# Performance work log

Hardware: AMD Instinct MI355X
Metric: run time of the kernel (lower is better)

The kernel has to match this reference:

```python
import jax, jax.numpy as jnp
import numpy as np
import math

B, S, D, H, NB = 32, 512, 512, 8, 2
DK = D // H
DF = 4 * D
EPS = 1e-8


def layer_norm(x, gamma, beta):
    # Matches torch: unbiased std (ddof=1), divide by (std + eps)
    mean = jnp.mean(x, axis=-1, keepdims=True)
    std = jnp.sqrt(jnp.var(x, axis=-1, keepdims=True, ddof=1))
    return gamma * (x - mean) / (std + EPS) + beta


def block(x, wq, bq, wk, bk, wv, bv, wr, br, ga, ba, wc1, bc1, wc2, bc2, gf, bf):
    # --- attention with ReLU-gated Q/K/V ---
    Q = jax.nn.relu(x @ wq.T + bq)  # [B,S,D]
    K = jax.nn.relu(x @ wk.T + bk)
    V = jax.nn.relu(x @ wv.T + bv)
    # chunk along last dim -> heads; head-major stacking is equivalent to this reshape
    Qh = Q.reshape(B, S, H, DK)
    Kh = K.reshape(B, S, H, DK)
    Vh = V.reshape(B, S, H, DK)
    scores = jnp.einsum('bqhd,bkhd->bhqk', Qh, Kh) / math.sqrt(DK)
    w = jax.nn.softmax(scores, axis=-1)
    out = jnp.einsum('bhqk,bkhd->bqhd', w, Vh).reshape(B, S, D)
    out = out + jax.nn.relu(x @ wr.T + br)
    out = layer_norm(out, ga, ba)
    # --- conv1d (kernel=1) feed-forward ---
    h = jax.nn.relu(out @ wc1.T + bc1)  # [B,S,4D]
    y = h @ wc2.T + bc2                 # [B,S,D]
    y = layer_norm(y + out, gf, bf)
    return y


def setup_inputs() -> dict:
    key = jax.random.key(0)
    ks = jax.random.split(key, 8)
    std = 0.01
    inp = {
        'x': jax.random.normal(ks[0], (B, S, D), jnp.float32),
        'wq': jax.random.normal(ks[1], (NB, D, D), jnp.float32) * std,
        'bq': jnp.zeros((NB, D), jnp.float32),
        'wk': jax.random.normal(ks[2], (NB, D, D), jnp.float32) * std,
        'bk': jnp.zeros((NB, D), jnp.float32),
        'wv': jax.random.normal(ks[3], (NB, D, D), jnp.float32) * std,
        'bv': jnp.zeros((NB, D), jnp.float32),
        'wr': jax.random.normal(ks[4], (NB, D, D), jnp.float32) * std,
        'br': jnp.zeros((NB, D), jnp.float32),
        'g_attn': jnp.ones((NB, D), jnp.float32),
        'b_attn': jnp.zeros((NB, D), jnp.float32),
        'wc1': jax.random.normal(ks[5], (NB, DF, D), jnp.float32) * (1.0 / math.sqrt(D)),
        'bc1': jnp.zeros((NB, DF), jnp.float32),
        'wc2': jax.random.normal(ks[6], (NB, D, DF), jnp.float32) * (1.0 / math.sqrt(DF)),
        'bc2': jnp.zeros((NB, D), jnp.float32),
        'g_ffn': jnp.ones((NB, D), jnp.float32),
        'b_ffn': jnp.zeros((NB, D), jnp.float32),
    }
    return inp


def reference(x, wq, bq, wk, bk, wv, bv, wr, br, g_attn, b_attn,
              wc1, bc1, wc2, bc2, g_ffn, b_ffn):
    enc = x
    for i in range(NB):
        enc = block(enc, wq[i], bq[i], wk[i], bk[i], wv[i], bv[i], wr[i], br[i],
                    g_attn[i], b_attn[i], wc1[i], bc1[i], wc2[i], bc2[i],
                    g_ffn[i], b_ffn[i])
    return enc
```

## Files before the change

### kernel.cpp

```cpp
#include <hip/hip_runtime.h>

typedef unsigned short u16;
typedef __bf16 bf16x8 __attribute__((ext_vector_type(8)));
typedef float f32x4 __attribute__((ext_vector_type(4)));
typedef unsigned short ushort8 __attribute__((ext_vector_type(8)));

__device__ __forceinline__ void gload_lds16(const void* g, void* l) {
  __builtin_amdgcn_global_load_lds(
      (const __attribute__((address_space(1))) void*)g,
      (__attribute__((address_space(3))) void*)l, 16, 0, 0);
}

__device__ __forceinline__ u16 f2bf(float f) {
  unsigned int u = __builtin_bit_cast(unsigned int, f);
  u = (u + 0x7fffu + ((u >> 16) & 1u)) >> 16;
  return (u16)u;
}
__device__ __forceinline__ u16 f2bf_trunc(float f) {
  return (u16)(__builtin_bit_cast(unsigned int, f) >> 16);
}
__device__ __forceinline__ float bf2f(u16 u) {
  unsigned int v = (unsigned int)u << 16;
  return __builtin_bit_cast(float, v);
}

__global__ void castk(const float* __restrict__ in, u16* __restrict__ out, int n,
                      float scale) {
  size_t i = ((size_t)blockIdx.x * 256 + threadIdx.x) * 8;
  if (i >= (size_t)n) return;
  const float4* p = (const float4*)(in + i);
  float4 a = p[0], b = p[1];
  ushort8 o;
  o[0] = f2bf(a.x * scale); o[1] = f2bf(a.y * scale);
  o[2] = f2bf(a.z * scale); o[3] = f2bf(a.w * scale);
  o[4] = f2bf(b.x * scale); o[5] = f2bf(b.y * scale);
  o[6] = f2bf(b.z * scale); o[7] = f2bf(b.w * scale);
  *(ushort8*)(out + i) = o;
}

__global__ void castw4(const float* __restrict__ w0, const float* __restrict__ w1,
                       const float* __restrict__ w2, const float* __restrict__ w3,
                       u16* __restrict__ out) {
  size_t idx = ((size_t)blockIdx.x * 256 + threadIdx.x) * 8;
  int i = (int)(idx >> 20);
  int j = (int)((idx >> 18) & 3);
  int e = (int)(idx & 262143);
  const float* src = (j == 0) ? w0 : (j == 1) ? w1 : (j == 2) ? w2 : w3;
  float scale = (j == 0) ? 0.125f : 1.0f;
  const float4* p = (const float4*)(src + (size_t)i * 262144 + e);
  float4 a = p[0], b = p[1];
  ushort8 o;
  o[0] = f2bf(a.x * scale); o[1] = f2bf(a.y * scale);
  o[2] = f2bf(a.z * scale); o[3] = f2bf(a.w * scale);
  o[4] = f2bf(b.x * scale); o[5] = f2bf(b.y * scale);
  o[6] = f2bf(b.z * scale); o[7] = f2bf(b.w * scale);
  *(ushort8*)(out + idx) = o;
}

__global__ void biasg(const float* __restrict__ b0, const float* __restrict__ b1,
                      const float* __restrict__ b2, const float* __restrict__ b3,
                      float* __restrict__ out) {
  int idx = blockIdx.x * 256 + threadIdx.x;
  int i = idx >> 11, j = (idx >> 9) & 3, c = idx & 511;
  const float* src = (j == 0) ? b0 : (j == 1) ? b1 : (j == 2) ? b2 : b3;
  float v = src[i * 512 + c];
  out[idx] = (j == 0) ? v * 0.125f : v;
}

template<int RELU, int WVT>
__global__ __launch_bounds__(256, 4)
void gemm97(const u16* __restrict__ A, const u16* __restrict__ W,
            const float* __restrict__ bias, u16* __restrict__ C,
            u16* __restrict__ VT, int M, int N, int K)
{
  __shared__ char lds[32768];
  char* ABase = lds;
  char* BBase = lds + 16384;

  const int tid = threadIdx.x, w = tid >> 6, l = tid & 63;
  const int l15 = l & 15, lh = l >> 4;
  const int nbn = N >> 7;
  const int p = blockIdx.x;
  const int bm = (p & 7) * 16 + (p >> 3) / nbn;
  const int bn = (p >> 3) % nbn;
  const int wm = w >> 1, wn = w & 1;
  const int NT = K >> 6;

  const int srow = l >> 3;
  const int scol = ((l & 7) ^ srow) << 3;
  const u16* aG = A + (size_t)(bm * 128 + srow) * K + scol;
  const u16* bG = W + (size_t)(bn * 128 + srow) * K + scol;

  auto stage = [&](int t) {
#pragma unroll
    for (int i = 0; i < 4; ++i) {
      int c = w * 4 + i;
      gload_lds16(aG + (size_t)(c * 8) * K + t * 64, ABase + c * 1024);
      gload_lds16(bG + (size_t)(c * 8) * K + t * 64, BBase + c * 1024);
    }
  };

  f32x4 acc[4][4] = {};

  for (int t = 0; t < NT; ++t) {
    __syncthreads();
    stage(t);
    __syncthreads();
    bf16x8 a[4], b[4];
#pragma unroll
    for (int kk = 0; kk < 2; ++kk) {
#pragma unroll
      for (int mf = 0; mf < 4; ++mf) {
        int row = wm * 64 + mf * 16 + l15;
        a[mf] = *(const bf16x8*)(ABase + row * 128 +
                 ((kk * 64 + lh * 16) ^ ((row & 7) << 4)));
      }
#pragma unroll
      for (int nf = 0; nf < 4; ++nf) {
        int row = wn * 64 + nf * 16 + l15;
        b[nf] = *(const bf16x8*)(BBase + row * 128 +
                 ((kk * 64 + lh * 16) ^ ((row & 7) << 4)));
      }
      __builtin_amdgcn_s_setprio(1);
#pragma unroll
      for (int mf = 0; mf < 4; ++mf)
#pragma unroll
        for (int nf = 0; nf < 4; ++nf)
          acc[mf][nf] = __builtin_amdgcn_mfma_f32_16x16x32_bf16(a[mf], b[nf], acc[mf][nf], 0, 0, 0);
      __builtin_amdgcn_s_setprio(0);
    }
  }

  __syncthreads();
  char* Ct = (char*)lds;
  const int rowL = wm * 64 + (lh << 2);
  const int colL = wn * 64 + l15;
  const bool dovt = WVT && (bn >= 8) && (bn < 12);
  float bv[4];
#pragma unroll
  for (int nf = 0; nf < 4; ++nf) bv[nf] = bias[bn * 128 + colL + nf * 16];

  if (!dovt) {
#pragma unroll
    for (int mf = 0; mf < 4; ++mf)
#pragma unroll
      for (int nf = 0; nf < 4; ++nf)
#pragma unroll
        for (int r = 0; r < 4; ++r) {
          float v = acc[mf][nf][r] + bv[nf];
          if (RELU) v = fmaxf(v, 0.f);
          int m = rowL + mf * 16 + r, n = colL + nf * 16;
          *(u16*)(Ct + m * 256 + ((n * 2) ^ ((m & 7) << 4))) = f2bf(v);
        }
    __syncthreads();
#pragma unroll
    for (int pass = 0; pass < 8; ++pass) {
      int row = pass * 16 + (tid >> 4);
      int c16 = tid & 15;
      bf16x8 vv = *(const bf16x8*)(Ct + row * 256 + ((c16 * 16) ^ ((row & 7) << 4)));
      *(bf16x8*)(&C[(size_t)(bm * 128 + row) * N + bn * 128 + c16 * 8]) = vv;
    }
  } else {
#pragma unroll
    for (int mf = 0; mf < 4; ++mf)
#pragma unroll
      for (int nf = 0; nf < 4; ++nf)
#pragma unroll
        for (int r = 0; r < 4; ++r) {
          float v = acc[mf][nf][r] + bv[nf];
          if (RELU) v = fmaxf(v, 0.f);
          int m = rowL + mf * 16 + r, d = colL + nf * 16;
          *(u16*)(Ct + d * 256 + ((m * 2) ^ ((d & 7) << 4))) = f2bf(v);
        }
    __syncthreads();
    const int batch = bm >> 2;
#pragma unroll
    for (int pass = 0; pass < 8; ++pass) {
      int dL = pass * 16 + (tid >> 4);
      int m16 = tid & 15;
      bf16x8 vv = *(const bf16x8*)(Ct + dL * 256 + ((m16 * 16) ^ ((dL & 7) << 4)));
      int head = (bn - 8) * 2 + (dL >> 6);
      int vtr = (batch * 8 + head) * 64 + (dL & 63);
      *(bf16x8*)(&VT[(size_t)vtr * 512 + (bm & 3) * 128 + m16 * 8]) = vv;
    }
  }
}

__global__ __launch_bounds__(256, 2)
void attn_kernel(const u16* __restrict__ qkvr, const u16* __restrict__ VT,
                 u16* __restrict__ F)
{
  const int D4 = 2048;
  __shared__ u16 Qs[128 * 64];
  __shared__ u16 Ks[2][64 * 64];
  __shared__ u16 Vs[2][64 * 64];
  __shared__ u16 Ps[128 * 64];

  const int tid = threadIdx.x, w = tid >> 6, l = tid & 63;
  const int bh = blockIdx.x & 255, qt = blockIdx.x >> 8;
  const int b = bh >> 3, h = bh & 7;
  const int lr = l >> 3, lc = ((l & 7) ^ lr) << 3;
  const int l15 = l & 15, lh = l >> 4;

  const u16* qG = qkvr + (size_t)(b * 512 + qt * 128) * D4 + h * 64 + lc;
#pragma unroll
  for (int i = 0; i < 4; ++i) {
    int c = w * 4 + i;
    gload_lds16(qG + (size_t)(c * 8 + lr) * D4, &Qs[c * 512]);
  }

  const u16* kG = qkvr + (size_t)(b * 512) * D4 + 512 + h * 64 + lc;
  const u16* vG = VT + (size_t)(bh * 64) * 512 + lc;

  auto stageKV = [&](int kt) {
    const int bsel = kt & 1;
#pragma unroll
    for (int i = 0; i < 2; ++i) {
      int c = w * 2 + i;
      gload_lds16(kG + (size_t)(kt * 64 + c * 8 + lr) * D4, &Ks[bsel][c * 512]);
      gload_lds16(vG + (size_t)(c * 8 + lr) * 512 + kt * 64, &Vs[bsel][c * 512]);
    }
  };
  stageKV(0);

  f32x4 o_acc[2][4] = {};
  float psum[2][4] = {};

  for (int kt = 0; kt < 8; ++kt) {
    __syncthreads();
    if (kt < 7) stageKV(kt + 1);
    const char* Kb = (const char*)Ks[kt & 1];
    const char* Vb = (const char*)Vs[kt & 1];

    f32x4 sacc[2][4] = {};
#pragma unroll
    for (int kk = 0; kk < 2; ++kk) {
      bf16x8 qa[2];
#pragma unroll
      for (int qq = 0; qq < 2; ++qq) {
        int qrow = w * 32 + qq * 16 + l15;
        qa[qq] = *(const bf16x8*)((const char*)Qs + qrow * 128 +
                  ((kk * 64 + (lh << 4)) ^ ((qrow & 7) << 4)));
      }
#pragma unroll
      for (int ni = 0; ni < 4; ++ni) {
        int krow = ni * 16 + l15;
        bf16x8 kb = *(const bf16x8*)(Kb + krow * 128 +
                    ((kk * 64 + (lh << 4)) ^ ((krow & 7) << 4)));
#pragma unroll
        for (int qq = 0; qq < 2; ++qq)
          sacc[qq][ni] = __builtin_amdgcn_mfma_f32_16x16x32_bf16(qa[qq], kb, sacc[qq][ni], 0, 0, 0);
      }
    }

#pragma unroll
    for (int qq = 0; qq < 2; ++qq)
#pragma unroll
      for (int r = 0; r < 4; ++r) {
        float p0 = __expf(sacc[qq][0][r]);
        float p1 = __expf(sacc[qq][1][r]);
        float p2 = __expf(sacc[qq][2][r]);
        float p3 = __expf(sacc[qq][3][r]);
        psum[qq][r] += (p0 + p1) + (p2 + p3);
        int q = w * 32 + qq * 16 + (lh << 2) + r;
        int sw = (q & 7) << 4;
        int col = l15 * 2;
        char* pb = (char*)Ps + q * 128;
        *(u16*)(pb + ((0  + col) ^ sw)) = f2bf_trunc(p0);
        *(u16*)(pb + ((32 + col) ^ sw)) = f2bf_trunc(p1);
        *(u16*)(pb + ((64 + col) ^ sw)) = f2bf_trunc(p2);
        *(u16*)(pb + ((96 + col) ^ sw)) = f2bf_trunc(p3);
      }

#pragma unroll
    for (int kk = 0; kk < 2; ++kk) {
      bf16x8 pa[2];
#pragma unroll
      for (int qq = 0; qq < 2; ++qq) {
        int qrow = w * 32 + qq * 16 + l15;
        pa[qq] = *(const bf16x8*)((const char*)Ps + qrow * 128 +
                  ((kk * 64 + (lh << 4)) ^ ((qrow & 7) << 4)));
      }
#pragma unroll
      for (int ni = 0; ni < 4; ++ni) {
        int d = ni * 16 + l15;
        bf16x8 vb = *(const bf16x8*)(Vb + d * 128 +
                    ((kk * 64 + (lh << 4)) ^ ((d & 7) << 4)));
#pragma unroll
        for (int qq = 0; qq < 2; ++qq)
          o_acc[qq][ni] = __builtin_amdgcn_mfma_f32_16x16x32_bf16(pa[qq], vb, o_acc[qq][ni], 0, 0, 0);
      }
    }
  }

  float lsum[2][4];
#pragma unroll
  for (int qq = 0; qq < 2; ++qq)
#pragma unroll
    for (int r = 0; r < 4; ++r) {
      float t = psum[qq][r];
#pragma unroll
      for (int m = 1; m < 16; m <<= 1) t += __shfl_xor(t, m);
      lsum[qq][r] = 1.f / t;
    }

#pragma unroll
  for (int qq = 0; qq < 2; ++qq)
#pragma unroll
    for (int ni = 0; ni < 4; ++ni) {
      int d = ni * 16 + l15;
#pragma unroll
      for (int r = 0; r < 4; ++r) {
        float v = o_acc[qq][ni][r] * lsum[qq][r];
        int q = w * 32 + qq * 16 + (lh << 2) + r;
        *(u16*)((char*)Ps + q * 128 + ((d * 2) ^ ((q & 7) << 4))) = f2bf(v);
      }
    }
  __syncthreads();
  const u16* Rbase = qkvr + (size_t)(b * 512 + qt * 128) * D4 + 1536 + h * 64;
  u16* Fbase = F + (size_t)(b * 512 + qt * 128) * 512 + h * 64;
#pragma unroll
  for (int pass = 0; pass < 4; ++pass) {
    int row = pass * 32 + (tid >> 3), c8 = tid & 7;
    ushort8 lv = *(const ushort8*)((char*)Ps + row * 128 + ((c8 * 16) ^ ((row & 7) << 4)));
    ushort8 rv = *(const ushort8*)(Rbase + (size_t)row * D4 + c8 * 8);
    ushort8 o;
#pragma unroll
    for (int j = 0; j < 8; ++j) o[j] = f2bf(bf2f(lv[j]) + bf2f(rv[j]));
    *(ushort8*)(Fbase + (size_t)row * 512 + c8 * 8) = o;
  }
}

template<int HAS_RES, int OUT_F32>
__global__ __launch_bounds__(256)
void ln_bf(const u16* __restrict__ in, const u16* __restrict__ res,
           const float* __restrict__ gamma, const float* __restrict__ beta,
           u16* __restrict__ outb, float* __restrict__ outf)
{
  const int l = threadIdx.x & 63;
  const size_t row = (size_t)blockIdx.x * 4 + (threadIdx.x >> 6);
  ushort8 iv = *(const ushort8*)(in + row * 512 + l * 8);
  float x[8];
#pragma unroll
  for (int j = 0; j < 8; ++j) x[j] = bf2f(iv[j]);
  if (HAS_RES) {
    ushort8 rv = *(const ushort8*)(res + row * 512 + l * 8);
#pragma unroll
    for (int j = 0; j < 8; ++j) x[j] += bf2f(rv[j]);
  }
  float s = 0.f, ss = 0.f;
#pragma unroll
  for (int j = 0; j < 8; ++j) { s += x[j]; ss += x[j] * x[j]; }
#pragma unroll
  for (int m = 1; m < 64; m <<= 1) { s += __shfl_xor(s, m); ss += __shfl_xor(ss, m); }
  float mean = s * (1.f / 512.f);
  float var = fmaxf((ss - 512.f * mean * mean) * (1.f / 511.f), 0.f);
  float inv = 1.f / (sqrtf(var) + 1e-8f);
  const float4* g4 = (const float4*)gamma;
  const float4* b4 = (const float4*)beta;
  float4 g0 = g4[l * 2], g1 = g4[l * 2 + 1];
  float4 b0 = b4[l * 2], b1 = b4[l * 2 + 1];
  float gg[8] = {g0.x, g0.y, g0.z, g0.w, g1.x, g1.y, g1.z, g1.w};
  float bb[8] = {b0.x, b0.y, b0.z, b0.w, b1.x, b1.y, b1.z, b1.w};
  float y[8];
#pragma unroll
  for (int j = 0; j < 8; ++j) y[j] = gg[j] * (x[j] - mean) * inv + bb[j];
  ushort8 o;
#pragma unroll
  for (int j = 0; j < 8; ++j) o[j] = f2bf(y[j]);
  *(ushort8*)(outb + row * 512 + l * 8) = o;
  if (OUT_F32) {
    float4* o4 = (float4*)(outf + row * 512);
    o4[l * 2]     = make_float4(y[0], y[1], y[2], y[3]);
    o4[l * 2 + 1] = make_float4(y[4], y[5], y[6], y[7]);
  }
}

extern "C" void kernel_launch(void* const* d_in, const int* in_sizes, int n_in,
                              void* d_out, int out_size, void* d_ws, size_t ws_size,
                              hipStream_t stream)
{
  const int B = 32, S = 512, D = 512, NB = 2, DF = 2048;
  const int M = B * S;

  const float* x   = (const float*)d_in[0];
  const float* ga  = (const float*)d_in[9];
  const float* ba  = (const float*)d_in[10];
  const float* wc1 = (const float*)d_in[11];
  const float* bc1 = (const float*)d_in[12];
  const float* wc2 = (const float*)d_in[13];
  const float* bc2 = (const float*)d_in[14];
  const float* gf  = (const float*)d_in[15];
  const float* bfp = (const float*)d_in[16];

  char* ws = (char*)d_ws;
  u16*   curb = (u16*)(ws + 0);
  u16*   qkvr = (u16*)(ws + 16777216);
  u16*   F    = (u16*)(ws + 83886080);
  u16*   Hg   = (u16*)(ws + 100663296);
  u16*   VT   = (u16*)(ws + 117440512);
  u16*   w4b  = (u16*)(ws + 134217728);
  u16*   wc1b = (u16*)(ws + 138412032);
  u16*   wc2b = (u16*)(ws + 142606336);
  float* b4   = (float*)(ws + 146800640);
  u16*   Ih   = qkvr;
  u16*   Y    = F;

  castk<<<M * D / 2048, 256, 0, stream>>>(x, curb, M * D, 1.0f);
  castw4<<<1024, 256, 0, stream>>>((const float*)d_in[1], (const float*)d_in[3],
                                   (const float*)d_in[5], (const float*)d_in[7], w4b);
  biasg<<<16, 256, 0, stream>>>((const float*)d_in[2], (const float*)d_in[4],
                                (const float*)d_in[6], (const float*)d_in[8], b4);
  castk<<<NB * DF * D / 2048, 256, 0, stream>>>(wc1, wc1b, NB * DF * D, 1.0f);
  castk<<<NB * DF * D / 2048, 256, 0, stream>>>(wc2, wc2b, NB * DF * D, 1.0f);

  for (int i = 0; i < NB; ++i) {
    const size_t wfo = (size_t)i * DF * D;
    gemm97<1, 1><<<128 * 16, 256, 0, stream>>>(curb, w4b + (size_t)i * 1048576,
                                               b4 + i * 2048, qkvr, VT, M, 2048, 512);
    attn_kernel<<<4 * 256, 256, 0, stream>>>(qkvr, VT, F);
    ln_bf<0, 0><<<M / 4, 256, 0, stream>>>(F, nullptr, ga + i * D, ba + i * D, Hg, nullptr);
    gemm97<1, 0><<<128 * 16, 256, 0, stream>>>(Hg, wc1b + wfo, bc1 + i * DF,
                                               Ih, nullptr, M, 2048, 512);
    gemm97<0, 0><<<128 * 4, 256, 0, stream>>>(Ih, wc2b + wfo, bc2 + i * D,
                                              Y, nullptr, M, 512, 2048);
    if (i == NB - 1)
      ln_bf<1, 1><<<M / 4, 256, 0, stream>>>(Y, Hg, gf + i * D, bfp + i * D,
                                             curb, (float*)d_out);
    else
      ln_bf<1, 0><<<M / 4, 256, 0, stream>>>(Y, Hg, gf + i * D, bfp + i * D,
                                             curb, nullptr);
  }
}
```

Before: 358.7 us.

## Add 256x256-tile 8-wave GEMM with phased LDS pipeline for QKV and FFN1

```diff
diff --git a/kernel.cpp b/kernel.cpp
--- a/kernel.cpp
+++ b/kernel.cpp
@@ -68,6 +68,175 @@
 }
 
 template<int RELU, int WVT>
+__global__ __launch_bounds__(512, 1)
+void gemm8p(const u16* __restrict__ A, const u16* __restrict__ W,
+            const float* __restrict__ bias, u16* __restrict__ C,
+            u16* __restrict__ VT, int M, int N, int K)
+{
+  __shared__ char lds[131072];
+
+  const int tid = threadIdx.x, w = tid >> 6, l = tid & 63;
+  const int l15 = l & 15, lh = l >> 4;
+  const int nbn = N >> 8;
+  const int p = blockIdx.x;
+  const int g0 = (p & 7) * ((gridDim.x >> 3) / nbn) * nbn + (p >> 3);
+  const int bm = g0 / nbn, bn = g0 % nbn;
+  const int wm = w >> 2, wn = w & 3;
+  const int NI = K >> 7;
+
+  const int srow = l >> 3;
+  const int scol = ((l & 7) ^ srow) << 3;
+
+  auto stA = [&](int t, int h) {
+#pragma unroll
+    for (int j = 0; j < 2; ++j) {
+      int c = w * 2 + j;
+      gload_lds16(A + (size_t)(bm * 256 + h * 128 + c * 8 + srow) * K + t * 64 + scol,
+                  lds + (t & 1) * 32768 + h * 16384 + c * 1024);
+    }
+  };
+  auto stB = [&](int t, int h) {
+#pragma unroll
+    for (int j = 0; j < 2; ++j) {
+      int c = w * 2 + j;
+      gload_lds16(W + (size_t)(bn * 256 + h * 128 + c * 8 + srow) * K + t * 64 + scol,
+                  lds + 65536 + (t & 1) * 32768 + h * 16384 + c * 1024);
+    }
+  };
+
+  f32x4 acc[8][4] = {};
+  bf16x8 a[2][8], b[2][4];
+
+  auto rdA = [&](int buf, int kk, bf16x8* dst) {
+#pragma unroll
+    for (int mf = 0; mf < 8; ++mf) {
+      int r = mf * 16 + l15;
+      dst[mf] = *(const bf16x8*)(lds + buf * 32768 + wm * 16384 + r * 128 +
+                 ((kk * 64 + lh * 16) ^ ((r & 7) << 4)));
+    }
+  };
+  auto rdB = [&](int buf, int kk, bf16x8* dst) {
+#pragma unroll
+    for (int nf = 0; nf < 4; ++nf) {
+      int r = (wn & 1) * 64 + nf * 16 + l15;
+      dst[nf] = *(const bf16x8*)(lds + 65536 + buf * 32768 + (wn >> 1) * 16384 +
+                 r * 128 + ((kk * 64 + lh * 16) ^ ((r & 7) << 4)));
+    }
+  };
+
+#define PH_MID()                                              \
+  __builtin_amdgcn_sched_barrier(0);                          \
+  __builtin_amdgcn_s_barrier();                               \
+  asm volatile("s_waitcnt lgkmcnt(0)" ::: "memory");          \
+  __builtin_amdgcn_sched_barrier(0)
+#define PH_END()                                              \
+  __builtin_amdgcn_sched_barrier(0);                          \
+  __builtin_amdgcn_s_barrier();                               \
+  __builtin_amdgcn_sched_barrier(0)
+#define QMFMA(KK, MH)                                         \
+  { __builtin_amdgcn_s_setprio(1);                            \
+    _Pragma("unroll") for (int mf = 0; mf < 4; ++mf)          \
+    _Pragma("unroll") for (int nf = 0; nf < 4; ++nf)          \
+      acc[(MH) * 4 + mf][nf] = __builtin_amdgcn_mfma_f32_16x16x32_bf16( \
+          a[KK][(MH) * 4 + mf], b[KK][nf], acc[(MH) * 4 + mf][nf], 0, 0, 0); \
+    __builtin_amdgcn_s_setprio(0); }
+
+  stA(0, 0); stA(0, 1); stB(0, 0); stB(0, 1); stA(1, 0); stA(1, 1);
+  asm volatile("s_waitcnt vmcnt(4)" ::: "memory");
+  __builtin_amdgcn_s_barrier();
+  __builtin_amdgcn_sched_barrier(0);
+
+  for (int i = 0; i < NI; ++i) {
+    const int t0 = 2 * i, t1 = 2 * i + 1;
+    const bool g = (i + 1 < NI);
+    rdA(0, 0, a[0]); rdB(0, 0, b[0]);
+    stB(t1, 0);
+    PH_MID(); QMFMA(0, 0); PH_END();
+    rdA(0, 1, a[1]); rdB(0, 1, b[1]);
+    stB(t1, 1);
+    PH_MID(); QMFMA(0, 1); PH_END();
+    if (g) stA(t0 + 2, 0);
+    PH_MID(); QMFMA(1, 0); PH_END();
+    if (g) stA(t0 + 2, 1);
+    PH_MID(); QMFMA(1, 1);
+    __builtin_amdgcn_sched_barrier(0);
+    if (g) asm volatile("s_waitcnt vmcnt(4)" ::: "memory");
+    else   asm volatile("s_waitcnt vmcnt(0)" ::: "memory");
+    PH_END();
+    rdA(1, 0, a[0]); rdB(1, 0, b[0]);
+    if (g) stB(t0 + 2, 0);
+    PH_MID(); QMFMA(0, 0); PH_END();
+    rdA(1, 1, a[1]); rdB(1, 1, b[1]);
+    if (g) stB(t0 + 2, 1);
+    PH_MID(); QMFMA(0, 1); PH_END();
+    if (g) stA(t0 + 3, 0);
+    PH_MID(); QMFMA(1, 0); PH_END();
+    if (g) stA(t0 + 3, 1);
+    PH_MID(); QMFMA(1, 1);
+    __builtin_amdgcn_sched_barrier(0);
+    if (g) asm volatile("s_waitcnt vmcnt(4)" ::: "memory");
+    PH_END();
+  }
+#undef PH_MID
+#undef PH_END
+#undef QMFMA
+
+  __syncthreads();
+  char* Ct = (char*)lds;
+  const int rowL = wm * 128 + (lh << 2);
+  const int colL = wn * 64 + l15;
+  const bool dovt = WVT && (bn == 4 || bn == 5);
+  float bv[4];
+#pragma unroll
+  for (int nf = 0; nf < 4; ++nf) bv[nf] = bias[bn * 256 + colL + nf * 16];
+
+  if (!dovt) {
+#pragma unroll
+    for (int mi = 0; mi < 8; ++mi)
+#pragma unroll
+      for (int nf = 0; nf < 4; ++nf)
+#pragma unroll
+        for (int r = 0; r < 4; ++r) {
+          float v = acc[mi][nf][r] + bv[nf];
+          if (RELU) v = fmaxf(v, 0.f);
+          int m = rowL + mi * 16 + r, n = colL + nf * 16;
+          *(u16*)(Ct + m * 512 + ((n * 2) ^ ((m & 7) << 4))) = f2bf(v);
+        }
+    __syncthreads();
+#pragma unroll
+    for (int pass = 0; pass < 16; ++pass) {
+      int row = pass * 16 + (tid >> 5);
+      int c16 = tid & 31;
+      bf16x8 vv = *(const bf16x8*)(Ct + row * 512 + ((c16 * 16) ^ ((row & 7) << 4)));
+      *(bf16x8*)(&C[(size_t)(bm * 256 + row) * N + bn * 256 + c16 * 8]) = vv;
+    }
+  } else {
+#pragma unroll
+    for (int mi = 0; mi < 8; ++mi)
+#pragma unroll
+      for (int nf = 0; nf < 4; ++nf)
+#pragma unroll
+        for (int r = 0; r < 4; ++r) {
+          float v = acc[mi][nf][r] + bv[nf];
+          if (RELU) v = fmaxf(v, 0.f);
+          int m = rowL + mi * 16 + r, d = colL + nf * 16;
+          *(u16*)(Ct + d * 512 + ((m * 2) ^ ((d & 7) << 4))) = f2bf(v);
+        }
+    __syncthreads();
+    const int batch = bm >> 1;
+#pragma unroll
+    for (int pass = 0; pass < 16; ++pass) {
+      int dL = pass * 16 + (tid >> 5);
+      int m16 = tid & 31;
+      bf16x8 vv = *(const bf16x8*)(Ct + dL * 512 + ((m16 * 16) ^ ((dL & 7) << 4)));
+      int head = (bn - 4) * 4 + (dL >> 6);
+      int vtr = (batch * 8 + head) * 64 + (dL & 63);
+      *(bf16x8*)(&VT[(size_t)vtr * 512 + (bm & 1) * 256 + m16 * 8]) = vv;
+    }
+  }
+}
+
+template<int RELU, int WVT>
 __global__ __launch_bounds__(256, 4)
 void gemm97(const u16* __restrict__ A, const u16* __restrict__ W,
             const float* __restrict__ bias, u16* __restrict__ C,
@@ -135,54 +304,28 @@
   char* Ct = (char*)lds;
   const int rowL = wm * 64 + (lh << 2);
   const int colL = wn * 64 + l15;
-  const bool dovt = WVT && (bn >= 8) && (bn < 12);
   float bv[4];
 #pragma unroll
   for (int nf = 0; nf < 4; ++nf) bv[nf] = bias[bn * 128 + colL + nf * 16];
 
-  if (!dovt) {
-#pragma unroll
-    for (int mf = 0; mf < 4; ++mf)
-#pragma unroll
-      for (int nf = 0; nf < 4; ++nf)
-#pragma unroll
-        for (int r = 0; r < 4; ++r) {
-          float v = acc[mf][nf][r] + bv[nf];
-          if (RELU) v = fmaxf(v, 0.f);
-          int m = rowL + mf * 16 + r, n = colL + nf * 16;
-          *(u16*)(Ct + m * 256 + ((n * 2) ^ ((m & 7) << 4))) = f2bf(v);
-        }
-    __syncthreads();
-#pragma unroll
-    for (int pass = 0; pass < 8; ++pass) {
-      int row = pass * 16 + (tid >> 4);
-      int c16 = tid & 15;
-      bf16x8 vv = *(const bf16x8*)(Ct + row * 256 + ((c16 * 16) ^ ((row & 7) << 4)));
-      *(bf16x8*)(&C[(size_t)(bm * 128 + row) * N + bn * 128 + c16 * 8]) = vv;
-    }
-  } else {
-#pragma unroll
-    for (int mf = 0; mf < 4; ++mf)
-#pragma unroll
-      for (int nf = 0; nf < 4; ++nf)
-#pragma unroll
-        for (int r = 0; r < 4; ++r) {
-          float v = acc[mf][nf][r] + bv[nf];
-          if (RELU) v = fmaxf(v, 0.f);
-          int m = rowL + mf * 16 + r, d = colL + nf * 16;
-          *(u16*)(Ct + d * 256 + ((m * 2) ^ ((d & 7) << 4))) = f2bf(v);
-        }
-    __syncthreads();
-    const int batch = bm >> 2;
-#pragma unroll
-    for (int pass = 0; pass < 8; ++pass) {
-      int dL = pass * 16 + (tid >> 4);
-      int m16 = tid & 15;
-      bf16x8 vv = *(const bf16x8*)(Ct + dL * 256 + ((m16 * 16) ^ ((dL & 7) << 4)));
-      int head = (bn - 8) * 2 + (dL >> 6);
-      int vtr = (batch * 8 + head) * 64 + (dL & 63);
-      *(bf16x8*)(&VT[(size_t)vtr * 512 + (bm & 3) * 128 + m16 * 8]) = vv;
-    }
+#pragma unroll
+  for (int mf = 0; mf < 4; ++mf)
+#pragma unroll
+    for (int nf = 0; nf < 4; ++nf)
+#pragma unroll
+      for (int r = 0; r < 4; ++r) {
+        float v = acc[mf][nf][r] + bv[nf];
+        if (RELU) v = fmaxf(v, 0.f);
+        int m = rowL + mf * 16 + r, n = colL + nf * 16;
+        *(u16*)(Ct + m * 256 + ((n * 2) ^ ((m & 7) << 4))) = f2bf(v);
+      }
+  __syncthreads();
+#pragma unroll
+  for (int pass = 0; pass < 8; ++pass) {
+    int row = pass * 16 + (tid >> 4);
+    int c16 = tid & 15;
+    bf16x8 vv = *(const bf16x8*)(Ct + row * 256 + ((c16 * 16) ^ ((row & 7) << 4)));
+    *(bf16x8*)(&C[(size_t)(bm * 128 + row) * N + bn * 128 + c16 * 8]) = vv;
   }
 }
 
@@ -416,12 +559,12 @@
 
   for (int i = 0; i < NB; ++i) {
     const size_t wfo = (size_t)i * DF * D;
-    gemm97<1, 1><<<128 * 16, 256, 0, stream>>>(curb, w4b + (size_t)i * 1048576,
-                                               b4 + i * 2048, qkvr, VT, M, 2048, 512);
+    gemm8p<1, 1><<<512, 512, 0, stream>>>(curb, w4b + (size_t)i * 1048576,
+                                          b4 + i * 2048, qkvr, VT, M, 2048, 512);
     attn_kernel<<<4 * 256, 256, 0, stream>>>(qkvr, VT, F);
     ln_bf<0, 0><<<M / 4, 256, 0, stream>>>(F, nullptr, ga + i * D, ba + i * D, Hg, nullptr);
-    gemm97<1, 0><<<128 * 16, 256, 0, stream>>>(Hg, wc1b + wfo, bc1 + i * DF,
-                                               Ih, nullptr, M, 2048, 512);
+    gemm8p<1, 0><<<512, 512, 0, stream>>>(Hg, wc1b + wfo, bc1 + i * DF,
+                                          Ih, nullptr, M, 2048, 512);
     gemm97<0, 0><<<128 * 4, 256, 0, stream>>>(Ih, wc2b + wfo, bc2 + i * D,
                                               Y, nullptr, M, 512, 2048);
     if (i == NB - 1)
```

New measurement: 478.2 us. 33.3% more time.

## Add double-buffered K=32 GEMM for QKV and FFN1, skip unused final bf16 output

Applied to the files above, without the earlier changes.

```diff
diff --git a/kernel.cpp b/kernel.cpp
--- a/kernel.cpp
+++ b/kernel.cpp
@@ -69,9 +69,128 @@
 
 template<int RELU, int WVT>
 __global__ __launch_bounds__(256, 4)
+void gemmDB(const u16* __restrict__ A, const u16* __restrict__ W,
+            const float* __restrict__ bias, u16* __restrict__ C,
+            u16* __restrict__ VT, int M, int N, int K)
+{
+  __shared__ char lds[32768];
+
+  const int tid = threadIdx.x, w = tid >> 6, l = tid & 63;
+  const int l15 = l & 15, lh = l >> 4;
+  const int nbn = N >> 7;
+  const int p = blockIdx.x;
+  const int bm = (p & 7) * 16 + (p >> 3) / nbn;
+  const int bn = (p >> 3) % nbn;
+  const int wm = w >> 1, wn = w & 1;
+  const int NT = K >> 5;
+
+  const int srow = l >> 2;
+  const int scol = ((l & 3) ^ ((l >> 3) & 3)) << 3;
+  const u16* aG = A + (size_t)(bm * 128 + srow) * K + scol;
+  const u16* bG = W + (size_t)(bn * 128 + srow) * K + scol;
+
+  auto stage = [&](int t) {
+    char* base = lds + (t & 1) * 16384;
+#pragma unroll
+    for (int i = 0; i < 2; ++i) {
+      int c = i * 4 + w;
+      gload_lds16(aG + (size_t)(c * 16) * K + t * 32, base + c * 1024);
+      gload_lds16(bG + (size_t)(c * 16) * K + t * 32, base + 8192 + c * 1024);
+    }
+  };
+
+  f32x4 acc[4][4] = {};
+  const int sw = ((l15 >> 1) & 3) << 4;
+
+  stage(0);
+  for (int t = 0; t < NT; ++t) {
+    asm volatile("s_waitcnt vmcnt(0)" ::: "memory");
+    __builtin_amdgcn_s_barrier();
+    __builtin_amdgcn_sched_barrier(0);
+    if (t + 1 < NT) stage(t + 1);
+
+    const char* Ab = lds + (t & 1) * 16384;
+    const char* Bb = Ab + 8192;
+    bf16x8 a[4], b[4];
+#pragma unroll
+    for (int mf = 0; mf < 4; ++mf) {
+      int row = wm * 64 + mf * 16 + l15;
+      a[mf] = *(const bf16x8*)(Ab + row * 64 + ((lh << 4) ^ sw));
+    }
+#pragma unroll
+    for (int nf = 0; nf < 4; ++nf) {
+      int row = wn * 64 + nf * 16 + l15;
+      b[nf] = *(const bf16x8*)(Bb + row * 64 + ((lh << 4) ^ sw));
+    }
+    __builtin_amdgcn_s_setprio(1);
+#pragma unroll
+    for (int mf = 0; mf < 4; ++mf)
+#pragma unroll
+      for (int nf = 0; nf < 4; ++nf)
+        acc[mf][nf] = __builtin_amdgcn_mfma_f32_16x16x32_bf16(a[mf], b[nf], acc[mf][nf], 0, 0, 0);
+    __builtin_amdgcn_s_setprio(0);
+  }
+
+  __syncthreads();
+  char* Ct = (char*)lds;
+  const int rowL = wm * 64 + (lh << 2);
+  const int colL = wn * 64 + l15;
+  const bool dovt = WVT && (bn >= 8) && (bn < 12);
+  float bv[4];
+#pragma unroll
+  for (int nf = 0; nf < 4; ++nf) bv[nf] = bias[bn * 128 + colL + nf * 16];
+
+  if (!dovt) {
+#pragma unroll
+    for (int mf = 0; mf < 4; ++mf)
+#pragma unroll
+      for (int nf = 0; nf < 4; ++nf)
+#pragma unroll
+        for (int r = 0; r < 4; ++r) {
+          float v = acc[mf][nf][r] + bv[nf];
+          if (RELU) v = fmaxf(v, 0.f);
+          int m = rowL + mf * 16 + r, n = colL + nf * 16;
+          *(u16*)(Ct + m * 256 + ((n * 2) ^ ((m & 7) << 4))) = f2bf(v);
+        }
+    __syncthreads();
+#pragma unroll
+    for (int pass = 0; pass < 8; ++pass) {
+      int row = pass * 16 + (tid >> 4);
+      int c16 = tid & 15;
+      bf16x8 vv = *(const bf16x8*)(Ct + row * 256 + ((c16 * 16) ^ ((row & 7) << 4)));
+      *(bf16x8*)(&C[(size_t)(bm * 128 + row) * N + bn * 128 + c16 * 8]) = vv;
+    }
+  } else {
+#pragma unroll
+    for (int mf = 0; mf < 4; ++mf)
+#pragma unroll
+      for (int nf = 0; nf < 4; ++nf)
+#pragma unroll
+        for (int r = 0; r < 4; ++r) {
+          float v = acc[mf][nf][r] + bv[nf];
+          if (RELU) v = fmaxf(v, 0.f);
+          int m = rowL + mf * 16 + r, d = colL + nf * 16;
+          *(u16*)(Ct + d * 256 + ((m * 2) ^ ((d & 7) << 4))) = f2bf(v);
+        }
+    __syncthreads();
+    const int batch = bm >> 2;
+#pragma unroll
+    for (int pass = 0; pass < 8; ++pass) {
+      int dL = pass * 16 + (tid >> 4);
+      int m16 = tid & 15;
+      bf16x8 vv = *(const bf16x8*)(Ct + dL * 256 + ((m16 * 16) ^ ((dL & 7) << 4)));
+      int head = (bn - 8) * 2 + (dL >> 6);
+      int vtr = (batch * 8 + head) * 64 + (dL & 63);
+      *(bf16x8*)(&VT[(size_t)vtr * 512 + (bm & 3) * 128 + m16 * 8]) = vv;
+    }
+  }
+}
+
+template<int RELU>
+__global__ __launch_bounds__(256, 4)
 void gemm97(const u16* __restrict__ A, const u16* __restrict__ W,
             const float* __restrict__ bias, u16* __restrict__ C,
-            u16* __restrict__ VT, int M, int N, int K)
+            int M, int N, int K)
 {
   __shared__ char lds[32768];
   char* ABase = lds;
@@ -135,54 +254,28 @@
   char* Ct = (char*)lds;
   const int rowL = wm * 64 + (lh << 2);
   const int colL = wn * 64 + l15;
-  const bool dovt = WVT && (bn >= 8) && (bn < 12);
   float bv[4];
 #pragma unroll
   for (int nf = 0; nf < 4; ++nf) bv[nf] = bias[bn * 128 + colL + nf * 16];
 
-  if (!dovt) {
-#pragma unroll
-    for (int mf = 0; mf < 4; ++mf)
-#pragma unroll
-      for (int nf = 0; nf < 4; ++nf)
-#pragma unroll
-        for (int r = 0; r < 4; ++r) {
-          float v = acc[mf][nf][r] + bv[nf];
-          if (RELU) v = fmaxf(v, 0.f);
-          int m = rowL + mf * 16 + r, n = colL + nf * 16;
-          *(u16*)(Ct + m * 256 + ((n * 2) ^ ((m & 7) << 4))) = f2bf(v);
-        }
-    __syncthreads();
-#pragma unroll
-    for (int pass = 0; pass < 8; ++pass) {
-      int row = pass * 16 + (tid >> 4);
-      int c16 = tid & 15;
-      bf16x8 vv = *(const bf16x8*)(Ct + row * 256 + ((c16 * 16) ^ ((row & 7) << 4)));
-      *(bf16x8*)(&C[(size_t)(bm * 128 + row) * N + bn * 128 + c16 * 8]) = vv;
-    }
-  } else {
-#pragma unroll
-    for (int mf = 0; mf < 4; ++mf)
-#pragma unroll
-      for (int nf = 0; nf < 4; ++nf)
-#pragma unroll
-        for (int r = 0; r < 4; ++r) {
-          float v = acc[mf][nf][r] + bv[nf];
-          if (RELU) v = fmaxf(v, 0.f);
-          int m = rowL + mf * 16 + r, d = colL + nf * 16;
-          *(u16*)(Ct + d * 256 + ((m * 2) ^ ((d & 7) << 4))) = f2bf(v);
-        }
-    __syncthreads();
-    const int batch = bm >> 2;
-#pragma unroll
-    for (int pass = 0; pass < 8; ++pass) {
-      int dL = pass * 16 + (tid >> 4);
-      int m16 = tid & 15;
-      bf16x8 vv = *(const bf16x8*)(Ct + dL * 256 + ((m16 * 16) ^ ((dL & 7) << 4)));
-      int head = (bn - 8) * 2 + (dL >> 6);
-      int vtr = (batch * 8 + head) * 64 + (dL & 63);
-      *(bf16x8*)(&VT[(size_t)vtr * 512 + (bm & 3) * 128 + m16 * 8]) = vv;
-    }
+#pragma unroll
+  for (int mf = 0; mf < 4; ++mf)
+#pragma unroll
+    for (int nf = 0; nf < 4; ++nf)
+#pragma unroll
+      for (int r = 0; r < 4; ++r) {
+        float v = acc[mf][nf][r] + bv[nf];
+        if (RELU) v = fmaxf(v, 0.f);
+        int m = rowL + mf * 16 + r, n = colL + nf * 16;
+        *(u16*)(Ct + m * 256 + ((n * 2) ^ ((m & 7) << 4))) = f2bf(v);
+      }
+  __syncthreads();
+#pragma unroll
+  for (int pass = 0; pass < 8; ++pass) {
+    int row = pass * 16 + (tid >> 4);
+    int c16 = tid & 15;
+    bf16x8 vv = *(const bf16x8*)(Ct + row * 256 + ((c16 * 16) ^ ((row & 7) << 4)));
+    *(bf16x8*)(&C[(size_t)(bm * 128 + row) * N + bn * 128 + c16 * 8]) = vv;
   }
 }
 
@@ -365,10 +458,12 @@
   float y[8];
 #pragma unroll
   for (int j = 0; j < 8; ++j) y[j] = gg[j] * (x[j] - mean) * inv + bb[j];
-  ushort8 o;
-#pragma unroll
-  for (int j = 0; j < 8; ++j) o[j] = f2bf(y[j]);
-  *(ushort8*)(outb + row * 512 + l * 8) = o;
+  if (outb) {
+    ushort8 o;
+#pragma unroll
+    for (int j = 0; j < 8; ++j) o[j] = f2bf(y[j]);
+    *(ushort8*)(outb + row * 512 + l * 8) = o;
+  }
   if (OUT_F32) {
     float4* o4 = (float4*)(outf + row * 512);
     o4[l * 2]     = make_float4(y[0], y[1], y[2], y[3]);
@@ -416,17 +511,17 @@
 
   for (int i = 0; i < NB; ++i) {
     const size_t wfo = (size_t)i * DF * D;
-    gemm97<1, 1><<<128 * 16, 256, 0, stream>>>(curb, w4b + (size_t)i * 1048576,
+    gemmDB<1, 1><<<128 * 16, 256, 0, stream>>>(curb, w4b + (size_t)i * 1048576,
                                                b4 + i * 2048, qkvr, VT, M, 2048, 512);
     attn_kernel<<<4 * 256, 256, 0, stream>>>(qkvr, VT, F);
     ln_bf<0, 0><<<M / 4, 256, 0, stream>>>(F, nullptr, ga + i * D, ba + i * D, Hg, nullptr);
-    gemm97<1, 0><<<128 * 16, 256, 0, stream>>>(Hg, wc1b + wfo, bc1 + i * DF,
+    gemmDB<1, 0><<<128 * 16, 256, 0, stream>>>(Hg, wc1b + wfo, bc1 + i * DF,
                                                Ih, nullptr, M, 2048, 512);
-    gemm97<0, 0><<<128 * 4, 256, 0, stream>>>(Ih, wc2b + wfo, bc2 + i * D,
-                                              Y, nullptr, M, 512, 2048);
+    gemm97<0><<<128 * 4, 256, 0, stream>>>(Ih, wc2b + wfo, bc2 + i * D,
+                                           Y, M, 512, 2048);
     if (i == NB - 1)
       ln_bf<1, 1><<<M / 4, 256, 0, stream>>>(Y, Hg, gf + i * D, bfp + i * D,
-                                             curb, (float*)d_out);
+                                             nullptr, (float*)d_out);
     else
       ln_bf<1, 0><<<M / 4, 256, 0, stream>>>(Y, Hg, gf + i * D, bfp + i * D,
                                              curb, nullptr);
```

Result: slower. 381.3 us (+6.3%).
